# Kernel optimization log

Hardware: AMD Instinct MI355X
Metric: run time of the kernel (lower is better)

The kernel has to match this reference:

```python
import math
import jax, jax.numpy as jnp
import numpy as np

B, S, D, H, DH = 4, 1024, 768, 24, 64  # batch, seq, d_model, n_heads (12*2), d_head
DG = 1  # d_gate


def setup_inputs() -> dict:
    key = jax.random.key(0)
    ks = jax.random.split(key, 12)
    sc = 0.02
    return {
        "x": jax.random.normal(ks[0], (B, S, D), dtype=jnp.float32),
        "W_Q": jax.random.normal(ks[1], (H, D, DH), dtype=jnp.float32) * sc,
        "W_K": jax.random.normal(ks[2], (H, D, DH), dtype=jnp.float32) * sc,
        "W_V": jax.random.normal(ks[3], (H, D, DH), dtype=jnp.float32) * sc,
        "W_O": jax.random.normal(ks[4], (H, DH, D), dtype=jnp.float32) * sc,
        "b_Q": jax.random.normal(ks[5], (H, DH), dtype=jnp.float32) * sc,
        "b_K": jax.random.normal(ks[6], (H, DH), dtype=jnp.float32) * sc,
        "b_V": jax.random.normal(ks[7], (H, DH), dtype=jnp.float32) * sc,
        "W_gate_Q": jax.random.normal(ks[8], (H, D, DG), dtype=jnp.float32) * sc,
        "W_gate_K": jax.random.normal(ks[9], (H, D, DG), dtype=jnp.float32) * sc,
        "b_gate_Q": jnp.zeros((H, DG), dtype=jnp.float32),
        "b_gate_K": jnp.zeros((H, DG), dtype=jnp.float32),
    }


def reference(x, W_Q, W_K, W_V, W_O, b_Q, b_K, b_V,
              W_gate_Q, W_gate_K, b_gate_Q, b_gate_K):
    eps = 1e-12
    # F.normalize: L2 over d_model axis (dim=1 of W_V, dim=2 of W_O)
    W_Vn = W_V / jnp.maximum(jnp.linalg.norm(W_V, axis=1, keepdims=True), eps)
    W_On = W_O / jnp.maximum(jnp.linalg.norm(W_O, axis=2, keepdims=True), eps)

    q = jnp.einsum('hmd,bqm->bqhd', W_Q, x) + b_Q            # [B,S,H,DH]
    k = jnp.einsum('hmd,bkm->bkhd', W_K, x) + b_K
    v = jnp.einsum('hmd,bkm->bkhd', W_Vn, x) + b_V
    qg = jnp.einsum('hmg,bqm->bqhg', W_gate_Q, x) + b_gate_Q  # [B,S,H,1]
    kg = jnp.einsum('hmg,bkm->bkhg', W_gate_K, x) + b_gate_K

    scores = jnp.einsum('bqhd,bkhd->bhqk', q, k)              # [B,H,S,S]
    gate = jnp.clip(jnp.einsum('bqhg,bkhg->bhqk', qg, kg), 0.0, 1.0)

    scaled = scores / math.sqrt(DH)
    causal = jnp.triu(jnp.ones((S, S), dtype=bool), 1)        # True above diagonal
    masked = jnp.where(causal[None, None], -jnp.inf, scaled)
    attn = jax.nn.softmax(masked, axis=-1)

    gated = gate * attn                                       # [B,H,S,S]
    # pre_z.sum(3) in the original == direct contraction over pos_k
    z = jnp.einsum('bhqk,bkhd->bhqd', gated, v)               # [B,H,S,DH]
    out = jnp.einsum('bhqd,hdm->bqm', z, W_On)                # sum over heads fused
    return out
```

## Files before the change

kernel.cpp:

```cpp
#include <hip/hip_runtime.h>
#include <math.h>


namespace {

typedef short bf16x8 __attribute__((ext_vector_type(8)));
typedef float f32x4 __attribute__((ext_vector_type(4)));
typedef unsigned short u16;
typedef u16 u16x8 __attribute__((ext_vector_type(8)));
typedef unsigned int u32;

constexpr int BB = 4, SS = 1024, DD = 768, HH = 24;
constexpr int RR = BB * SS;
constexpr int NC = HH * 64;
constexpr int NQKV = 3 * NC;
constexpr int NTOT = NQKV + 128;

__device__ inline u16 f2bf(float f) {
    u32 u = __float_as_uint(f);
    u += 0x7FFFu + ((u >> 16) & 1u);
    return (u16)(u >> 16);
}

__device__ __forceinline__ void async16(const void* g, const void* lds) {
    __builtin_amdgcn_global_load_lds(
        (const __attribute__((address_space(1))) u32*)(unsigned long long)(size_t)g,
        (__attribute__((address_space(3))) u32*)(u32)(size_t)lds, 16, 0, 0);
}

__global__ __launch_bounds__(256)
void norms_kernel(const float* __restrict__ Wv, const float* __restrict__ Wo,
                  float* __restrict__ invV, float* __restrict__ invO) {
    int j = blockIdx.x;
    int h = j >> 6, dh = j & 63;
    __shared__ float sv[256], so[256];
    float av = 0.f, ao = 0.f;
    for (int d = threadIdx.x; d < DD; d += 256) {
        float a = Wv[(h * DD + d) * 64 + dh];
        av += a * a;
        float b = Wo[(size_t)j * DD + d];
        ao += b * b;
    }
    sv[threadIdx.x] = av; so[threadIdx.x] = ao;
    __syncthreads();
    for (int s = 128; s > 0; s >>= 1) {
        if (threadIdx.x < s) {
            sv[threadIdx.x] += sv[threadIdx.x + s];
            so[threadIdx.x] += so[threadIdx.x + s];
        }
        __syncthreads();
    }
    if (threadIdx.x == 0) {
        invV[j] = 1.f / fmaxf(sqrtf(sv[0]), 1e-12f);
        invO[j] = 1.f / fmaxf(sqrtf(so[0]), 1e-12f);
    }
}

__global__ __launch_bounds__(256)
void x2bf_kernel(const float* __restrict__ x, u16* __restrict__ xb) {
    int idx = blockIdx.x * 256 + threadIdx.x;
    float4 v = ((const float4*)x)[idx];
    ushort4 o;
    o.x = f2bf(v.x); o.y = f2bf(v.y); o.z = f2bf(v.z); o.w = f2bf(v.w);
    ((ushort4*)xb)[idx] = o;
}

__global__ __launch_bounds__(256)
void pack_wqkv_kernel(const float* __restrict__ Wq, const float* __restrict__ Wk,
                      const float* __restrict__ Wv, const float* __restrict__ invV,
                      u16* __restrict__ wT) {
    const int k0 = blockIdx.x * 64, h = blockIdx.y, p = blockIdx.z;
    const float* W = (p == 0 ? Wq : p == 1 ? Wk : Wv) + (size_t)h * DD * 64;
    __shared__ float sT[64][68];
    const int t = threadIdx.x;
#pragma unroll
    for (int rep = 0; rep < 4; rep++) {
        int idx = t + rep * 256; int kk = idx >> 4, c = idx & 15;
        *(float4*)&sT[kk][c * 4] = *(const float4*)&W[(size_t)(k0 + kk) * 64 + c * 4];
    }
    __syncthreads();
#pragma unroll
    for (int rep = 0; rep < 2; rep++) {
        int idx = t + rep * 256; int dh = idx >> 3, cj = idx & 7;
        float sc = (p == 2) ? invV[h * 64 + dh] : 1.f;
        u16x8 o;
#pragma unroll
        for (int i = 0; i < 8; i++) o[i] = f2bf(sT[cj * 8 + i][dh] * sc);
        *(u16x8*)&wT[(size_t)(p * NC + h * 64 + dh) * DD + k0 + cj * 8] = o;
    }
}

__global__ __launch_bounds__(256)
void pack_gates_kernel(const float* __restrict__ Wgq, const float* __restrict__ Wgk,
                       u16* __restrict__ wT) {
    int g = blockIdx.x;
    u16* dst = wT + (size_t)(NQKV + g) * DD;
    if (g < 48) {
        const float* src = ((g & 1) ? Wgk : Wgq) + (size_t)(g >> 1) * DD;
        for (int c = threadIdx.x; c < DD; c += 256) dst[c] = f2bf(src[c]);
    } else {
        for (int c = threadIdx.x; c < DD; c += 256) dst[c] = 0;
    }
}

__global__ void pack_bias_kernel(const float* __restrict__ bq, const float* __restrict__ bk,
                                 const float* __restrict__ bv, float* __restrict__ biasp) {
    int n = blockIdx.x * 256 + threadIdx.x;
    if (n >= NQKV) return;
    int p = n / NC, rem = n % NC;
    biasp[n] = (p == 0) ? bq[rem] : (p == 1) ? bk[rem] : bv[rem];
}

__global__ __launch_bounds__(256)
void pack_wo_kernel(const float* __restrict__ Wo, u16* __restrict__ woT) {
    const int j0 = blockIdx.x * 64, d0 = blockIdx.y * 64;
    __shared__ float sT[64][68];
    const int t = threadIdx.x;
#pragma unroll
    for (int rep = 0; rep < 4; rep++) {
        int idx = t + rep * 256; int jj = idx >> 4, c = idx & 15;
        *(float4*)&sT[jj][c * 4] = *(const float4*)&Wo[(size_t)(j0 + jj) * DD + d0 + c * 4];
    }
    __syncthreads();
#pragma unroll
    for (int rep = 0; rep < 2; rep++) {
        int idx = t + rep * 256; int dd = idx >> 3, cj = idx & 7;
        u16x8 o;
#pragma unroll
        for (int i = 0; i < 8; i++) o[i] = f2bf(sT[cj * 8 + i][dd]);
        *(u16x8*)&woT[(size_t)(d0 + dd) * NC + j0 + cj * 8] = o;
    }
}

__global__ __launch_bounds__(256)
void qkv_gemm_kernel(const u16* __restrict__ xb, const u16* __restrict__ wT,
                     const float* __restrict__ biasp,
                     const float* __restrict__ bgq, const float* __restrict__ bgk,
                     u16* __restrict__ qo, u16* __restrict__ ko, u16* __restrict__ vto,
                     float* __restrict__ qgo, float* __restrict__ kgo) {
    const int n0 = blockIdx.x * 128, row0 = blockIdx.y * 128;
    const int t = threadIdx.x, w = t >> 6, l = t & 63, lr = l & 15, lq = l >> 4;
    const int wr = (w >> 1) * 64, wc = (w & 1) * 64;
    __shared__ u16 smem[4 * 4608];
    u16* sA = smem;
    u16* sB = smem + 8192;

    const int src_row = l >> 3;
    const int cbs = (l & 7) ^ src_row;
    const int swz = lr & 7;

    f32x4 acc[4][4] = {};
    for (int k0 = 0; k0 < DD; k0 += 64) {
        __syncthreads();
#pragma unroll
        for (int i = 0; i < 4; i++) {
            int ch = w * 4 + i;
            int rowA = ch * 8 + src_row;
            async16(xb + (size_t)(row0 + rowA) * DD + k0 + cbs * 8, sA + ch * 512);
            async16(wT + (size_t)(n0 + rowA) * DD + k0 + cbs * 8, sB + ch * 512);
        }
        __syncthreads();
#pragma unroll
        for (int s = 0; s < 2; s++) {
            const int j8 = ((s * 4 + lq) ^ swz) * 8;
            bf16x8 af[4], bf[4];
#pragma unroll
            for (int i = 0; i < 4; i++) {
                af[i] = *(const bf16x8*)&sA[(wr + i * 16 + lr) * 64 + j8];
                bf[i] = *(const bf16x8*)&sB[(wc + i * 16 + lr) * 64 + j8];
            }
#pragma unroll
            for (int mt = 0; mt < 4; mt++)
#pragma unroll
                for (int nt = 0; nt < 4; nt++)
                    acc[mt][nt] = __builtin_amdgcn_mfma_f32_16x16x32_bf16(
                        af[mt], bf[nt], acc[mt][nt], 0, 0, 0);
        }
    }
    __syncthreads();

    const int p = n0 / NC;
    const int b = row0 >> 10, s0 = row0 & (SS - 1);

    if (p == 3) {
        if (wc == 0) {
#pragma unroll
            for (int nt = 0; nt < 3; nt++) {
                int j = nt * 16 + lr, hh = j >> 1;
                float bias = (j & 1) ? bgk[hh] : bgq[hh];
                float* dst = (j & 1) ? kgo : qgo;
#pragma unroll
                for (int mt = 0; mt < 4; mt++)
#pragma unroll
                    for (int r = 0; r < 4; r++)
                        dst[((size_t)b * HH + hh) * SS + s0 + wr + mt * 16 + lq * 4 + r] =
                            acc[mt][nt][r] + bias;
            }
        }
        return;
    }

    const int cq = n0 + wc, srow = s0 + wr;
    u16* tw = smem + w * 4608;
    float bb[4];
#pragma unroll
    for (int nt = 0; nt < 4; nt++) bb[nt] = biasp[cq + nt * 16 + lr];

    if (p < 2) {
        const float sc = (p == 0) ? 0.125f : 1.f;
#pragma unroll
        for (int mt = 0; mt < 4; mt++)
#pragma unroll
            for (int nt = 0; nt < 4; nt++)
#pragma unroll
                for (int r = 0; r < 4; r++)
                    tw[(mt * 16 + lq * 4 + r) * 72 + nt * 16 + lr] =
                        f2bf((acc[mt][nt][r] + bb[nt]) * sc);
        const int h = (cq - p * NC) >> 6;
        u16* dst = (p == 0 ? qo : ko) + ((size_t)(b * HH + h) * SS + srow) * 64;
#pragma unroll
        for (int c = 0; c < 8; c++)
            *(u16x8*)&dst[(size_t)l * 64 + c * 8] = *(const u16x8*)&tw[l * 72 + c * 8];
    } else {
#pragma unroll
        for (int mt = 0; mt < 4; mt++)
#pragma unroll
            for (int nt = 0; nt < 4; nt++)
#pragma unroll
                for (int r = 0; r < 4; r++)
                    tw[(nt * 16 + lr) * 72 + mt * 16 + lq * 4 + r] =
                        f2bf(acc[mt][nt][r] + bb[nt]);
        const int h = (cq - 2 * NC) >> 6;
        u16* dst = vto + ((size_t)(b * HH + h) * 64 + l) * SS + srow;
#pragma unroll
        for (int c = 0; c < 8; c++)
            *(u16x8*)&dst[c * 8] = *(const u16x8*)&tw[l * 72 + c * 8];
    }
}

__global__ __launch_bounds__(256)
void attn_kernel(const u16* __restrict__ qb, const u16* __restrict__ kb,
                 const u16* __restrict__ vtb, const float* __restrict__ qg,
                 const float* __restrict__ kg, const float* __restrict__ invO,
                 u16* __restrict__ z) {
    const int pr = blockIdx.x, h = blockIdx.y, b = blockIdx.z;
    const int t = threadIdx.x, w = t >> 6, l = t & 63, lr = l & 15, lq = l >> 4;

    __shared__ u16 sK[2][64 * 64], sVT[2][64 * 64];
    __shared__ u16 sP[4][16 * 72];
    u16* tP = sP[w];

    const size_t bh = (size_t)(b * HH + h);
    const u16* Kb = kb + bh * SS * 64;
    const u16* Vt = vtb + bh * 64 * SS;
    const float* kgb = kg + bh * SS;

    const int src_row = l >> 3;
    const int cbs = (l & 7) ^ src_row;
    const int swz = lr & 7;

    auto stage = [&](int kt, int buf) {
#pragma unroll
        for (int i = 0; i < 2; i++) {
            int kc = w * 2 + i;
            int row = kc * 8 + src_row;
            async16(Kb + ((size_t)(kt * 64 + row)) * 64 + cbs * 8, sK[buf] + kc * 512);
            async16(Vt + (size_t)row * SS + kt * 64 + cbs * 8, sVT[buf] + kc * 512);
        }
    };

    stage(0, 0);
    int cur = 0;
#pragma unroll
    for (int sub = 0; sub < 2; sub++) {
        const int QT = sub ? (15 - pr) : pr;
        const int q0 = QT * 64 + w * 16;
        const u16* Qw = qb + (bh * SS + q0) * 64;
        bf16x8 aq0 = *(const bf16x8*)(Qw + (size_t)lr * 64 + lq * 8);
        bf16x8 aq1 = *(const bf16x8*)(Qw + (size_t)lr * 64 + 32 + lq * 8);
        float qgr[4];
#pragma unroll
        for (int r = 0; r < 4; r++) qgr[r] = qg[bh * SS + q0 + lq * 4 + r];

        f32x4 o[4] = {};
        float lacc[4] = {};

        for (int kt = 0; kt <= QT; kt++) {
            __syncthreads();
            if (kt < QT) stage(kt + 1, cur ^ 1);
            else if (sub == 0) stage(0, cur ^ 1);
            const u16* K_ = sK[cur];
            const u16* V_ = sVT[cur];

            float kgv[4];
#pragma unroll
            for (int nt = 0; nt < 4; nt++) kgv[nt] = kgb[kt * 64 + nt * 16 + lr];

            f32x4 sf[4] = {};
#pragma unroll
            for (int s = 0; s < 2; s++) {
                const int j8 = ((s * 4 + lq) ^ swz) * 8;
                const bf16x8 aqs = s ? aq1 : aq0;
#pragma unroll
                for (int nt = 0; nt < 4; nt++) {
                    bf16x8 bk = *(const bf16x8*)&K_[(nt * 16 + lr) * 64 + j8];
                    sf[nt] = __builtin_amdgcn_mfma_f32_16x16x32_bf16(aqs, bk, sf[nt], 0, 0, 0);
                }
            }
            if (kt == QT) {
#pragma unroll
                for (int nt = 0; nt < 4; nt++)
#pragma unroll
                    for (int r = 0; r < 4; r++)
                        if (nt * 16 + lr > w * 16 + lq * 4 + r) sf[nt][r] = -INFINITY;
            }

#pragma unroll
            for (int nt = 0; nt < 4; nt++)
#pragma unroll
                for (int r = 0; r < 4; r++) {
                    float pv = __expf(sf[nt][r]);
                    lacc[r] += pv;
                    float g = fminf(fmaxf(qgr[r] * kgv[nt], 0.f), 1.f);
                    tP[(lq * 4 + r) * 72 + nt * 16 + lr] = f2bf(pv * g);
                }

#pragma unroll
            for (int c = 0; c < 2; c++) {
                bf16x8 ap = *(const bf16x8*)&tP[lr * 72 + c * 32 + lq * 8];
                const int j8 = ((c * 4 + lq) ^ swz) * 8;
#pragma unroll
                for (int dt = 0; dt < 4; dt++) {
                    bf16x8 bv = *(const bf16x8*)&V_[(dt * 16 + lr) * 64 + j8];
                    o[dt] = __builtin_amdgcn_mfma_f32_16x16x32_bf16(ap, bv, o[dt], 0, 0, 0);
                }
            }
            cur ^= 1;
        }

#pragma unroll
        for (int r = 0; r < 4; r++) {
            float v = lacc[r];
            v += __shfl_xor(v, 1);
            v += __shfl_xor(v, 2);
            v += __shfl_xor(v, 4);
            v += __shfl_xor(v, 8);
            lacc[r] = __builtin_amdgcn_rcpf(v);
        }

        const int col0 = h * 64;
#pragma unroll
        for (int dt = 0; dt < 4; dt++) {
            float io = invO[col0 + dt * 16 + lr];
#pragma unroll
            for (int r = 0; r < 4; r++) {
                float val = o[dt][r] * lacc[r] * io;
                z[((size_t)b * SS + q0 + lq * 4 + r) * NC + col0 + dt * 16 + lr] = f2bf(val);
            }
        }
    }
}

__global__ __launch_bounds__(256)
void out_gemm_kernel(const u16* __restrict__ zb, const u16* __restrict__ woT,
                     float* __restrict__ out) {
    const int n0 = blockIdx.x * 64, row0 = blockIdx.y * 64;
    const int t = threadIdx.x, w = t >> 6, l = t & 63, lr = l & 15, lq = l >> 4;
    const int wr = (w >> 1) * 32, wc = (w & 1) * 32;
    __shared__ u16 sA[2][64 * 64], sB[2][64 * 64];

    const int src_row = l >> 3;
    const int cbs = (l & 7) ^ src_row;
    const int swz = lr & 7;

    auto stage = [&](int k0, int buf) {
#pragma unroll
        for (int i = 0; i < 2; i++) {
            int ch = w * 2 + i;
            int row = ch * 8 + src_row;
            async16(zb + (size_t)(row0 + row) * NC + k0 + cbs * 8, sA[buf] + ch * 512);
            async16(woT + (size_t)(n0 + row) * NC + k0 + cbs * 8, sB[buf] + ch * 512);
        }
    };

    stage(0, 0);
    int cur = 0;
    f32x4 acc[2][2] = {};
    for (int k0 = 0; k0 < NC; k0 += 64) {
        __syncthreads();
        if (k0 + 64 < NC) stage(k0 + 64, cur ^ 1);
#pragma unroll
        for (int s = 0; s < 2; s++) {
            const int j8 = ((s * 4 + lq) ^ swz) * 8;
            bf16x8 af[2], bf[2];
#pragma unroll
            for (int i = 0; i < 2; i++) {
                af[i] = *(const bf16x8*)&sA[cur][(wr + i * 16 + lr) * 64 + j8];
                bf[i] = *(const bf16x8*)&sB[cur][(wc + i * 16 + lr) * 64 + j8];
            }
#pragma unroll
            for (int mt = 0; mt < 2; mt++)
#pragma unroll
                for (int nt = 0; nt < 2; nt++)
                    acc[mt][nt] = __builtin_amdgcn_mfma_f32_16x16x32_bf16(
                        af[mt], bf[nt], acc[mt][nt], 0, 0, 0);
        }
        cur ^= 1;
    }
#pragma unroll
    for (int mt = 0; mt < 2; mt++)
#pragma unroll
        for (int nt = 0; nt < 2; nt++)
#pragma unroll
            for (int r = 0; r < 4; r++)
                out[(size_t)(row0 + wr + mt * 16 + lq * 4 + r) * DD + n0 + wc + nt * 16 + lr] =
                    acc[mt][nt][r];
}

}

extern "C" void kernel_launch(void* const* d_in, const int* in_sizes, int n_in,
                              void* d_out, int out_size, void* d_ws, size_t ws_size,
                              hipStream_t stream) {
    const float* x   = (const float*)d_in[0];
    const float* W_Q = (const float*)d_in[1];
    const float* W_K = (const float*)d_in[2];
    const float* W_V = (const float*)d_in[3];
    const float* W_O = (const float*)d_in[4];
    const float* b_Q = (const float*)d_in[5];
    const float* b_K = (const float*)d_in[6];
    const float* b_V = (const float*)d_in[7];
    const float* Wgq = (const float*)d_in[8];
    const float* Wgk = (const float*)d_in[9];
    const float* bgq = (const float*)d_in[10];
    const float* bgk = (const float*)d_in[11];
    float* out = (float*)d_out;

    char* wsb = (char*)d_ws;
    auto alloc = [&](size_t bytes) -> char* {
        char* p = wsb;
        wsb += (bytes + 255) & ~(size_t)255;
        return p;
    };
    float* invV  = (float*)alloc((size_t)NC * 4);
    float* invO  = (float*)alloc((size_t)NC * 4);
    float* biasp = (float*)alloc((size_t)NQKV * 4);
    float* qg    = (float*)alloc((size_t)RR * HH * 4);
    float* kg    = (float*)alloc((size_t)RR * HH * 4);
    u16* xb      = (u16*)alloc((size_t)RR * DD * 2);
    u16* wT      = (u16*)alloc((size_t)NTOT * DD * 2);
    u16* woT     = (u16*)alloc((size_t)DD * NC * 2);
    u16* qb      = (u16*)alloc((size_t)RR * 64 * HH * 2);
    u16* kb      = (u16*)alloc((size_t)RR * 64 * HH * 2);
    u16* vtb     = (u16*)alloc((size_t)RR * 64 * HH * 2);
    u16* zb      = (u16*)alloc((size_t)RR * NC * 2);

    norms_kernel<<<NC, 256, 0, stream>>>(W_V, W_O, invV, invO);
    x2bf_kernel<<<RR * DD / 4 / 256, 256, 0, stream>>>(x, xb);
    pack_wqkv_kernel<<<dim3(DD / 64, HH, 3), 256, 0, stream>>>(W_Q, W_K, W_V, invV, wT);
    pack_gates_kernel<<<128, 256, 0, stream>>>(Wgq, Wgk, wT);
    pack_bias_kernel<<<(NQKV + 255) / 256, 256, 0, stream>>>(b_Q, b_K, b_V, biasp);
    pack_wo_kernel<<<dim3(NC / 64, DD / 64), 256, 0, stream>>>(W_O, woT);
    qkv_gemm_kernel<<<dim3(NTOT / 128, RR / 128), 256, 0, stream>>>(
        xb, wT, biasp, bgq, bgk, qb, kb, vtb, qg, kg);
    attn_kernel<<<dim3(8, HH, BB), 256, 0, stream>>>(
        qb, kb, vtb, qg, kg, invO, zb);
    out_gemm_kernel<<<dim3(DD / 64, RR / 64), 256, 0, stream>>>(zb, woT, out);
}
```

Measured before the change: 231.1 us.

## Keep attention probabilities in registers via transposed score MFMA, exp2 scaling

The score MFMA is computed transposed (K as A operand), so each lane holds a probability layout that feeds directly as the A fragment of 16x16x16 MFMAs for P·V. This removes the per-wave LDS round trip for P and its barriers-free stores/loads. Q is pre-scaled by log2(e)/8 so exp2f can be used, the causal mask is applied after the exponential, and row sums are reduced with fewer shuffles. The QKV GEMM grid is remapped into row groups for L2 reuse and the attention grid puts heads fastest, which changes block ordering and cache locality. The trade-off is twice as many smaller MFMAs for P·V and narrower V loads from LDS.

```diff
diff --git a/kernel.cpp b/kernel.cpp
--- a/kernel.cpp
+++ b/kernel.cpp
@@ -5,6 +5,7 @@
 namespace {
 
 typedef short bf16x8 __attribute__((ext_vector_type(8)));
+typedef short bf16x4 __attribute__((ext_vector_type(4)));
 typedef float f32x4 __attribute__((ext_vector_type(4)));
 typedef unsigned short u16;
 typedef u16 u16x8 __attribute__((ext_vector_type(8)));
@@ -138,7 +139,11 @@
                      const float* __restrict__ bgq, const float* __restrict__ bgk,
                      u16* __restrict__ qo, u16* __restrict__ ko, u16* __restrict__ vto,
                      float* __restrict__ qgo, float* __restrict__ kgo) {
-    const int n0 = blockIdx.x * 128, row0 = blockIdx.y * 128;
+    const int flat = blockIdx.x + 37 * blockIdx.y;
+    const int grp = flat / 296;
+    const int rem = flat - grp * 296;
+    const int row0 = (grp * 8 + (rem & 7)) * 128;
+    const int n0 = (rem >> 3) * 128;
     const int t = threadIdx.x, w = t >> 6, l = t & 63, lr = l & 15, lq = l >> 4;
     const int wr = (w >> 1) * 64, wc = (w & 1) * 64;
     __shared__ u16 smem[4 * 4608];
@@ -207,7 +212,7 @@
     for (int nt = 0; nt < 4; nt++) bb[nt] = biasp[cq + nt * 16 + lr];
 
     if (p < 2) {
-        const float sc = (p == 0) ? 0.125f : 1.f;
+        const float sc = (p == 0) ? 0.18033688f : 1.f;
 #pragma unroll
         for (int mt = 0; mt < 4; mt++)
 #pragma unroll
@@ -243,12 +248,10 @@
                  const u16* __restrict__ vtb, const float* __restrict__ qg,
                  const float* __restrict__ kg, const float* __restrict__ invO,
                  u16* __restrict__ z) {
-    const int pr = blockIdx.x, h = blockIdx.y, b = blockIdx.z;
+    const int h = blockIdx.x, b = blockIdx.y, pr = blockIdx.z;
     const int t = threadIdx.x, w = t >> 6, l = t & 63, lr = l & 15, lq = l >> 4;
 
     __shared__ u16 sK[2][64 * 64], sVT[2][64 * 64];
-    __shared__ u16 sP[4][16 * 72];
-    u16* tP = sP[w];
 
     const size_t bh = (size_t)(b * HH + h);
     const u16* Kb = kb + bh * SS * 64;
@@ -278,12 +281,10 @@
         const u16* Qw = qb + (bh * SS + q0) * 64;
         bf16x8 aq0 = *(const bf16x8*)(Qw + (size_t)lr * 64 + lq * 8);
         bf16x8 aq1 = *(const bf16x8*)(Qw + (size_t)lr * 64 + 32 + lq * 8);
-        float qgr[4];
-#pragma unroll
-        for (int r = 0; r < 4; r++) qgr[r] = qg[bh * SS + q0 + lq * 4 + r];
+        const float qgr = qg[bh * SS + q0 + lr];
 
         f32x4 o[4] = {};
-        float lacc[4] = {};
+        float lacc = 0.f;
 
         for (int kt = 0; kt <= QT; kt++) {
             __syncthreads();
@@ -292,11 +293,12 @@
             const u16* K_ = sK[cur];
             const u16* V_ = sVT[cur];
 
-            float kgv[4];
-#pragma unroll
-            for (int nt = 0; nt < 4; nt++) kgv[nt] = kgb[kt * 64 + nt * 16 + lr];
-
-            f32x4 sf[4] = {};
+            float4 kgv[4];
+#pragma unroll
+            for (int nt = 0; nt < 4; nt++)
+                kgv[nt] = *(const float4*)&kgb[kt * 64 + nt * 16 + lq * 4];
+
+            f32x4 st[4] = {};
 #pragma unroll
             for (int s = 0; s < 2; s++) {
                 const int j8 = ((s * 4 + lq) ^ swz) * 8;
@@ -304,49 +306,44 @@
 #pragma unroll
                 for (int nt = 0; nt < 4; nt++) {
                     bf16x8 bk = *(const bf16x8*)&K_[(nt * 16 + lr) * 64 + j8];
-                    sf[nt] = __builtin_amdgcn_mfma_f32_16x16x32_bf16(aqs, bk, sf[nt], 0, 0, 0);
+                    st[nt] = __builtin_amdgcn_mfma_f32_16x16x32_bf16(bk, aqs, st[nt], 0, 0, 0);
                 }
             }
-            if (kt == QT) {
-#pragma unroll
-                for (int nt = 0; nt < 4; nt++)
-#pragma unroll
-                    for (int r = 0; r < 4; r++)
-                        if (nt * 16 + lr > w * 16 + lq * 4 + r) sf[nt][r] = -INFINITY;
-            }
-
-#pragma unroll
-            for (int nt = 0; nt < 4; nt++)
+
+            const bool diag = (kt == QT);
+            bf16x4 af[4];
+#pragma unroll
+            for (int nt = 0; nt < 4; nt++) {
 #pragma unroll
                 for (int r = 0; r < 4; r++) {
-                    float pv = __expf(sf[nt][r]);
-                    lacc[r] += pv;
-                    float g = fminf(fmaxf(qgr[r] * kgv[nt], 0.f), 1.f);
-                    tP[(lq * 4 + r) * 72 + nt * 16 + lr] = f2bf(pv * g);
+                    float pv = exp2f(st[nt][r]);
+                    if (diag && (nt * 16 + lq * 4 + r > w * 16 + lr)) pv = 0.f;
+                    lacc += pv;
+                    float g = fminf(fmaxf(qgr * ((const float*)&kgv[nt])[r], 0.f), 1.f);
+                    af[nt][r] = (short)f2bf(pv * g);
                 }
-
-#pragma unroll
-            for (int c = 0; c < 2; c++) {
-                bf16x8 ap = *(const bf16x8*)&tP[lr * 72 + c * 32 + lq * 8];
-                const int j8 = ((c * 4 + lq) ^ swz) * 8;
+            }
+
+#pragma unroll
+            for (int nt = 0; nt < 4; nt++) {
+                const int vcol = (((nt * 2 + (lq >> 1)) ^ swz) << 3) + ((lq & 1) << 2);
 #pragma unroll
                 for (int dt = 0; dt < 4; dt++) {
-                    bf16x8 bv = *(const bf16x8*)&V_[(dt * 16 + lr) * 64 + j8];
-                    o[dt] = __builtin_amdgcn_mfma_f32_16x16x32_bf16(ap, bv, o[dt], 0, 0, 0);
+                    bf16x4 vf = *(const bf16x4*)&V_[(dt * 16 + lr) * 64 + vcol];
+                    o[dt] = __builtin_amdgcn_mfma_f32_16x16x16bf16_1k(af[nt], vf, o[dt], 0, 0, 0);
                 }
             }
             cur ^= 1;
         }
 
-#pragma unroll
-        for (int r = 0; r < 4; r++) {
-            float v = lacc[r];
-            v += __shfl_xor(v, 1);
-            v += __shfl_xor(v, 2);
-            v += __shfl_xor(v, 4);
-            v += __shfl_xor(v, 8);
-            lacc[r] = __builtin_amdgcn_rcpf(v);
-        }
+        float lv = lacc;
+        lv += __shfl_xor(lv, 16);
+        lv += __shfl_xor(lv, 32);
+        const float linv = __builtin_amdgcn_rcpf(lv);
+        float inv_r[4];
+#pragma unroll
+        for (int r = 0; r < 4; r++)
+            inv_r[r] = __shfl(linv, (l & 48) | (lq * 4 + r));
 
         const int col0 = h * 64;
 #pragma unroll
@@ -354,7 +351,7 @@
             float io = invO[col0 + dt * 16 + lr];
 #pragma unroll
             for (int r = 0; r < 4; r++) {
-                float val = o[dt][r] * lacc[r] * io;
+                float val = o[dt][r] * inv_r[r] * io;
                 z[((size_t)b * SS + q0 + lq * 4 + r) * NC + col0 + dt * 16 + lr] = f2bf(val);
             }
         }
@@ -463,7 +460,7 @@
     pack_wo_kernel<<<dim3(NC / 64, DD / 64), 256, 0, stream>>>(W_O, woT);
     qkv_gemm_kernel<<<dim3(NTOT / 128, RR / 128), 256, 0, stream>>>(
         xb, wT, biasp, bgq, bgk, qb, kb, vtb, qg, kg);
-    attn_kernel<<<dim3(8, HH, BB), 256, 0, stream>>>(
+    attn_kernel<<<dim3(HH, BB, 8), 256, 0, stream>>>(
         qb, kb, vtb, qg, kg, invO, zb);
     out_gemm_kernel<<<dim3(DD / 64, RR / 64), 256, 0, stream>>>(zb, woT, out);
 }
```

Measured after the change: 233.2 us. No clear change (+0.9%).
